# Kernel optimization log

Measured on AMD Instinct MI355X. Metric: run time of the kernel, lower is better.

Reference implementation:

```python
import jax, jax.numpy as jnp
import numpy as np

N_NODES = 50000
N_EDGES = 600000
HIDDEN = 128


def setup_inputs() -> dict:
    key = jax.random.key(0)
    ks = jax.random.split(key, 8)
    x = jax.random.normal(ks[0], (N_NODES, HIDDEN), dtype=jnp.float32)
    edge_index = jax.random.randint(ks[1], (2, N_EDGES), 0, N_NODES, dtype=jnp.int32)
    s = 1.0 / np.sqrt(HIDDEN)
    # PyG SAGEConv: lin_l applied to aggregated neighbors (with bias), lin_r to root (no bias)
    W1l = jax.random.uniform(ks[2], (HIDDEN, HIDDEN), jnp.float32, -s, s)
    b1l = jax.random.uniform(ks[3], (HIDDEN,), jnp.float32, -s, s)
    W1r = jax.random.uniform(ks[4], (HIDDEN, HIDDEN), jnp.float32, -s, s)
    W2l = jax.random.uniform(ks[5], (HIDDEN, HIDDEN), jnp.float32, -s, s)
    b2l = jax.random.uniform(ks[6], (HIDDEN,), jnp.float32, -s, s)
    W2r = jax.random.uniform(ks[7], (HIDDEN, HIDDEN), jnp.float32, -s, s)
    return {"x": x, "edge_index": edge_index, "W1l": W1l, "b1l": b1l,
            "W1r": W1r, "W2l": W2l, "b2l": b2l, "W2r": W2r}


def _sage_conv(x, src, dst, Wl, bl, Wr):
    # mean aggregation of source features at destination nodes
    msg_sum = jax.ops.segment_sum(x[src], dst, num_segments=N_NODES)  # [N, H]
    deg = jax.ops.segment_sum(jnp.ones((src.shape[0],), x.dtype), dst,
                              num_segments=N_NODES)  # [N]
    agg = msg_sum / jnp.maximum(deg, 1.0)[:, None]
    return agg @ Wl.T + bl + x @ Wr.T


def reference(x, edge_index, W1l, b1l, W1r, W2l, b2l, W2r):
    src, dst = edge_index[0], edge_index[1]
    h = jax.nn.relu(_sage_conv(x, src, dst, W1l, b1l, W1r))
    out = _sage_conv(h, src, dst, W2l, b2l, W2r)
    return out
```

## Files before the change

kernel.cpp:

```cpp
#include <hip/hip_runtime.h>
#include <hip/hip_bf16.h>

#define N_NODES 50000
#define N_EDGES 600000
#define HID 128
#define SCAN_BLOCKS ((N_NODES + 255) / 256)

typedef __attribute__((ext_vector_type(8))) __bf16 bf16x8;
typedef __attribute__((ext_vector_type(4))) float f32x4;

static __device__ __forceinline__ unsigned short f2b(float v) {
    return __builtin_bit_cast(unsigned short, (__bf16)v);
}


__global__ void k_deg(const int* __restrict__ dst, int* __restrict__ fill, int ne) {
    int e = blockIdx.x * blockDim.x + threadIdx.x;
    if (e < ne) atomicAdd(&fill[dst[e]], 1);
}

__global__ __launch_bounds__(256) void k_bsum(const int* __restrict__ fill, int* __restrict__ bsum, int n) {
    __shared__ int s[256];
    int tid = threadIdx.x;
    int i = blockIdx.x * 256 + tid;
    s[tid] = (i < n) ? fill[i] : 0;
    __syncthreads();
#pragma unroll
    for (int off = 128; off > 0; off >>= 1) {
        if (tid < off) s[tid] += s[tid + off];
        __syncthreads();
    }
    if (tid == 0) bsum[blockIdx.x] = s[0];
}

__global__ __launch_bounds__(256) void k_scan_bsum(int* __restrict__ bsum, int* __restrict__ row_off,
                                                   int nb, int n) {
    __shared__ int s[256];
    int tid = threadIdx.x;
    int v = (tid < nb) ? bsum[tid] : 0;
    s[tid] = v;
    __syncthreads();
#pragma unroll
    for (int off = 1; off < 256; off <<= 1) {
        int t = (tid >= off) ? s[tid - off] : 0;
        __syncthreads();
        s[tid] += t;
        __syncthreads();
    }
    if (tid < nb) bsum[tid] = s[tid] - v;
    if (tid == 255) row_off[n] = s[255];
}

__global__ __launch_bounds__(256) void k_write_off(int* __restrict__ fill, const int* __restrict__ bsum,
                                                   int* __restrict__ row_off, float* __restrict__ inv_deg,
                                                   int n) {
    __shared__ int s[256];
    int tid = threadIdx.x;
    int i = blockIdx.x * 256 + tid;
    int c = (i < n) ? fill[i] : 0;
    s[tid] = c;
    __syncthreads();
#pragma unroll
    for (int off = 1; off < 256; off <<= 1) {
        int t = (tid >= off) ? s[tid - off] : 0;
        __syncthreads();
        s[tid] += t;
        __syncthreads();
    }
    if (i < n) {
        row_off[i] = bsum[blockIdx.x] + s[tid] - c;
        inv_deg[i] = 1.0f / (float)max(c, 1);
        fill[i] = 0;
    }
}

__global__ void k_place(const int* __restrict__ src, const int* __restrict__ dst,
                        const int* __restrict__ row_off, int* __restrict__ fill,
                        int* __restrict__ csr, int ne) {
    int e = blockIdx.x * blockDim.x + threadIdx.x;
    if (e < ne) {
        int d = dst[e];
        int pos = atomicAdd(&fill[d], 1);
        csr[row_off[d] + pos] = src[e];
    }
}


__global__ void k_cast(const float* __restrict__ x, unsigned short* __restrict__ xb, int n4) {
    int i = blockIdx.x * blockDim.x + threadIdx.x;
    if (i >= n4) return;
    float4 v = *(const float4*)(x + (size_t)i * 4);
    ushort4 o;
    o.x = f2b(v.x); o.y = f2b(v.y); o.z = f2b(v.z); o.w = f2b(v.w);
    *(ushort4*)(xb + (size_t)i * 4) = o;
}


__global__ void k_prepV(const float* __restrict__ W1l, const float* __restrict__ W1r,
                        const float* __restrict__ W2l, const float* __restrict__ W2r,
                        unsigned short* __restrict__ V1, unsigned short* __restrict__ V2) {
    int idx = blockIdx.x * blockDim.x + threadIdx.x;
    if (idx >= 2 * 128 * 256) return;
    int which = idx >> 15;
    int i = idx & 32767;
    int j = i >> 8, k = i & 255;
    const float* Wl = which ? W2l : W1l;
    const float* Wr = which ? W2r : W1r;
    float v = (k < HID) ? Wl[j * HID + k] : Wr[j * HID + k - HID];
    (which ? V2 : V1)[i] = f2b(v);
}


static __device__ __forceinline__ void acc_bf2(uint2 v, float& a0, float& a1, float& a2, float& a3) {
    a0 += __uint_as_float(v.x << 16);
    a1 += __uint_as_float(v.x & 0xffff0000u);
    a2 += __uint_as_float(v.y << 16);
    a3 += __uint_as_float(v.y & 0xffff0000u);
}

__global__ __launch_bounds__(256) void k_agg(const unsigned short* __restrict__ xb,
                                             const int* __restrict__ csr,
                                             const int* __restrict__ row_off,
                                             const float* __restrict__ inv_deg,
                                             unsigned short* __restrict__ aggB, int n) {
    int g = (blockIdx.x * blockDim.x + threadIdx.x) >> 5;
    int lane = threadIdx.x & 31;
    if (g >= n) return;
    int e0 = row_off[g], e1 = row_off[g + 1];
    float a0 = 0.f, a1 = 0.f, a2 = 0.f, a3 = 0.f;
    int e = e0;
    for (; e + 4 <= e1; e += 4) {
        int s0 = csr[e + 0];
        int s1 = csr[e + 1];
        int s2 = csr[e + 2];
        int s3 = csr[e + 3];
        uint2 v0 = *(const uint2*)(xb + (size_t)s0 * HID + lane * 4);
        uint2 v1 = *(const uint2*)(xb + (size_t)s1 * HID + lane * 4);
        uint2 v2 = *(const uint2*)(xb + (size_t)s2 * HID + lane * 4);
        uint2 v3 = *(const uint2*)(xb + (size_t)s3 * HID + lane * 4);
        acc_bf2(v0, a0, a1, a2, a3);
        acc_bf2(v1, a0, a1, a2, a3);
        acc_bf2(v2, a0, a1, a2, a3);
        acc_bf2(v3, a0, a1, a2, a3);
    }
    if (e + 2 <= e1) {
        int s0 = csr[e + 0];
        int s1 = csr[e + 1];
        uint2 v0 = *(const uint2*)(xb + (size_t)s0 * HID + lane * 4);
        uint2 v1 = *(const uint2*)(xb + (size_t)s1 * HID + lane * 4);
        acc_bf2(v0, a0, a1, a2, a3);
        acc_bf2(v1, a0, a1, a2, a3);
        e += 2;
    }
    if (e < e1) {
        int s0 = csr[e];
        uint2 v0 = *(const uint2*)(xb + (size_t)s0 * HID + lane * 4);
        acc_bf2(v0, a0, a1, a2, a3);
    }
    float inv = inv_deg[g];
    ushort4 o;
    o.x = f2b(a0 * inv); o.y = f2b(a1 * inv); o.z = f2b(a2 * inv); o.w = f2b(a3 * inv);
    *(ushort4*)(aggB + (size_t)g * HID + lane * 4) = o;
}


__global__ __launch_bounds__(512) void k_gemm(const unsigned short* __restrict__ aggB,
                                              const unsigned short* __restrict__ xinB,
                                              const unsigned short* __restrict__ VT,
                                              const float* __restrict__ bias,
                                              float* __restrict__ outF,
                                              unsigned short* __restrict__ outB,
                                              int mode ,
                                              int nrows) {
    __shared__ char As[32768];
    __shared__ char Bs[32768];
    int tid = threadIdx.x;
    int w = tid >> 6, l = tid & 63;
    int r0 = blockIdx.x * 128;

    f32x4 acc[8] = {};

    int arow = w * 16 + (l & 15);
    int kgrp = (l >> 4) * 8;

    for (int p = 0; p < 2; ++p) {
        const unsigned short* Asrc = p ? xinB : aggB;
#pragma unroll
        for (int q = 0; q < 4; ++q) {
            int c = tid + q * 512;
            int m = c >> 4, c16 = c & 15;
            int gr = r0 + m;
            uint4 v = make_uint4(0, 0, 0, 0);
            if (gr < nrows) v = *(const uint4*)(Asrc + (size_t)gr * HID + c16 * 8);
            int byt = (m * 256 + c16 * 16) ^ ((m & 7) << 4);
            *(uint4*)(As + byt) = v;
        }
#pragma unroll
        for (int q = 0; q < 4; ++q) {
            int c = tid + q * 512;
            int j = c >> 4, c16 = c & 15;
            uint4 v = *(const uint4*)(VT + (size_t)j * 256 + p * 128 + c16 * 8);
            int byt = (j * 256 + c16 * 16) ^ ((j & 7) << 4);
            *(uint4*)(Bs + byt) = v;
        }
        __syncthreads();

#pragma unroll
        for (int s = 0; s < 4; ++s) {
            int koff = (s * 32 + kgrp) * 2;
            bf16x8 a = *(const bf16x8*)(As + ((arow * 256 + koff) ^ ((arow & 7) << 4)));
#pragma unroll
            for (int cc = 0; cc < 8; ++cc) {
                int brow = cc * 16 + (l & 15);
                bf16x8 b = *(const bf16x8*)(Bs + ((brow * 256 + koff) ^ ((brow & 7) << 4)));
                acc[cc] = __builtin_amdgcn_mfma_f32_16x16x32_bf16(a, b, acc[cc], 0, 0, 0);
            }
        }
        __syncthreads();
    }

    int lo = l & 15, hi = l >> 4;
#pragma unroll
    for (int cc = 0; cc < 8; ++cc) {
        int col = cc * 16 + lo;
        float bv = bias[col];
#pragma unroll
        for (int i = 0; i < 4; ++i) {
            int gr = r0 + w * 16 + hi * 4 + i;
            if (gr < nrows) {
                float v = acc[cc][i] + bv;
                if (mode) {
                    v = fmaxf(v, 0.f);
                    outB[(size_t)gr * HID + col] = f2b(v);
                } else {
                    outF[(size_t)gr * HID + col] = v;
                }
            }
        }
    }
}


extern "C" void kernel_launch(void* const* d_in, const int* in_sizes, int n_in,
                              void* d_out, int out_size, void* d_ws, size_t ws_size,
                              hipStream_t stream) {
    const float* x   = (const float*)d_in[0];
    const int*   ei  = (const int*)d_in[1];
    const float* W1l = (const float*)d_in[2];
    const float* b1l = (const float*)d_in[3];
    const float* W1r = (const float*)d_in[4];
    const float* W2l = (const float*)d_in[5];
    const float* b2l = (const float*)d_in[6];
    const float* W2r = (const float*)d_in[7];
    float* out = (float*)d_out;

    const int* src = ei;
    const int* dst = ei + N_EDGES;

    char* w = (char*)d_ws;
    unsigned short* aggB = (unsigned short*)(w);
    unsigned short* buf0 = (unsigned short*)(w + 12800000);
    int*   csr     = (int*)(w + 25600000);
    int*   row_off = (int*)(w + 28000000);
    int*   fill    = (int*)(w + 28200192);
    float* inv_deg = (float*)(w + 28400384);
    unsigned short* V1 = (unsigned short*)(w + 28600576);
    unsigned short* V2 = (unsigned short*)(w + 28666112);
    int*   bsum    = (int*)(w + 28731648);

    hipMemsetAsync(fill, 0, N_NODES * sizeof(int), stream);
    k_deg<<<(N_EDGES + 255) / 256, 256, 0, stream>>>(dst, fill, N_EDGES);
    k_bsum<<<SCAN_BLOCKS, 256, 0, stream>>>(fill, bsum, N_NODES);
    k_scan_bsum<<<1, 256, 0, stream>>>(bsum, row_off, SCAN_BLOCKS, N_NODES);
    k_write_off<<<SCAN_BLOCKS, 256, 0, stream>>>(fill, bsum, row_off, inv_deg, N_NODES);
    k_place<<<(N_EDGES + 255) / 256, 256, 0, stream>>>(src, dst, row_off, fill, csr, N_EDGES);

    k_prepV<<<(2 * 128 * 256 + 255) / 256, 256, 0, stream>>>(W1l, W1r, W2l, W2r, V1, V2);
    k_cast<<<(N_NODES * HID / 4 + 255) / 256, 256, 0, stream>>>(x, buf0, N_NODES * HID / 4);

    const int gemm_grid = (N_NODES + 127) / 128;

    k_agg<<<(N_NODES * 32 + 255) / 256, 256, 0, stream>>>(buf0, csr, row_off, inv_deg, aggB, N_NODES);
    k_gemm<<<gemm_grid, 512, 0, stream>>>(aggB, buf0, V1, b1l, out, buf0, 1, N_NODES);

    k_agg<<<(N_NODES * 32 + 255) / 256, 256, 0, stream>>>(buf0, csr, row_off, inv_deg, aggB, N_NODES);
    k_gemm<<<gemm_grid, 512, 0, stream>>>(aggB, buf0, V2, b2l, out, buf0, 0, N_NODES);
}
```

Baseline: 165.9 us.

## Fuse neighbor aggregation into GEMM and merge prep and scan kernels

New measurement: 297.8 us. 1.79x slower.

```diff
diff --git a/kernel.cpp b/kernel.cpp
--- a/kernel.cpp
+++ b/kernel.cpp
@@ -4,13 +4,59 @@
 #define N_NODES 50000
 #define N_EDGES 600000
 #define HID 128
-#define SCAN_BLOCKS ((N_NODES + 255) / 256)
 
 typedef __attribute__((ext_vector_type(8))) __bf16 bf16x8;
 typedef __attribute__((ext_vector_type(4))) float f32x4;
 
 static __device__ __forceinline__ unsigned short f2b(float v) {
     return __builtin_bit_cast(unsigned short, (__bf16)v);
+}
+
+
+#define NCAST (N_NODES * HID / 8)
+#define NVT   (2 * 128 * 256 / 8)
+#define NFILL (N_NODES / 4)
+#define NPREP (NCAST + NVT + NFILL)
+
+__global__ __launch_bounds__(256) void k_prep(const float* __restrict__ x,
+                                              const float* __restrict__ W1l, const float* __restrict__ W1r,
+                                              const float* __restrict__ W2l, const float* __restrict__ W2r,
+                                              unsigned short* __restrict__ xb,
+                                              unsigned short* __restrict__ V1,
+                                              unsigned short* __restrict__ V2,
+                                              int* __restrict__ fill) {
+    int idx = blockIdx.x * 256 + threadIdx.x;
+    if (idx < NCAST) {
+        const float4* xp = (const float4*)(x + (size_t)idx * 8);
+        float4 a = xp[0], b = xp[1];
+        uint4 o;
+        o.x = f2b(a.x) | ((unsigned)f2b(a.y) << 16);
+        o.y = f2b(a.z) | ((unsigned)f2b(a.w) << 16);
+        o.z = f2b(b.x) | ((unsigned)f2b(b.y) << 16);
+        o.w = f2b(b.z) | ((unsigned)f2b(b.w) << 16);
+        *(uint4*)(xb + (size_t)idx * 8) = o;
+    } else if (idx < NCAST + NVT) {
+        int t = idx - NCAST;
+        int i0 = t * 8;
+        int which = i0 >> 15;
+        const float* Wl = which ? W2l : W1l;
+        const float* Wr = which ? W2r : W1r;
+        unsigned short* V = which ? V2 : V1;
+        int ii = i0 & 32767;
+        int j = ii >> 8, k0 = ii & 255;
+        const float* Wp = (k0 < HID) ? (Wl + j * HID + k0) : (Wr + j * HID + (k0 - HID));
+        const float4* wp4 = (const float4*)Wp;
+        float4 a = wp4[0], b = wp4[1];
+        uint4 o;
+        o.x = f2b(a.x) | ((unsigned)f2b(a.y) << 16);
+        o.y = f2b(a.z) | ((unsigned)f2b(a.w) << 16);
+        o.z = f2b(b.x) | ((unsigned)f2b(b.y) << 16);
+        o.w = f2b(b.z) | ((unsigned)f2b(b.w) << 16);
+        *(uint4*)(V + ii) = o;
+    } else if (idx < NPREP) {
+        int z = idx - (NCAST + NVT);
+        *(int4*)(fill + z * 4) = make_int4(0, 0, 0, 0);
+    }
 }
 
 
@@ -19,59 +65,33 @@
     if (e < ne) atomicAdd(&fill[dst[e]], 1);
 }
 
-__global__ __launch_bounds__(256) void k_bsum(const int* __restrict__ fill, int* __restrict__ bsum, int n) {
-    __shared__ int s[256];
+#define SCAN_T 1024
+#define SCAN_PER ((N_NODES + SCAN_T - 1) / SCAN_T)
+
+__global__ __launch_bounds__(1024) void k_scan1(int* __restrict__ fill, int* __restrict__ row_off,
+                                                float* __restrict__ inv_deg, int n) {
+    __shared__ int s[SCAN_T];
     int tid = threadIdx.x;
-    int i = blockIdx.x * 256 + tid;
-    s[tid] = (i < n) ? fill[i] : 0;
-    __syncthreads();
-#pragma unroll
-    for (int off = 128; off > 0; off >>= 1) {
-        if (tid < off) s[tid] += s[tid + off];
-        __syncthreads();
-    }
-    if (tid == 0) bsum[blockIdx.x] = s[0];
-}
-
-__global__ __launch_bounds__(256) void k_scan_bsum(int* __restrict__ bsum, int* __restrict__ row_off,
-                                                   int nb, int n) {
-    __shared__ int s[256];
-    int tid = threadIdx.x;
-    int v = (tid < nb) ? bsum[tid] : 0;
-    s[tid] = v;
-    __syncthreads();
-#pragma unroll
-    for (int off = 1; off < 256; off <<= 1) {
+    int s0 = tid * SCAN_PER, s1 = min(s0 + SCAN_PER, n);
+    int sum = 0;
+    for (int i = s0; i < s1; ++i) sum += fill[i];
+    s[tid] = sum;
+    __syncthreads();
+    for (int off = 1; off < SCAN_T; off <<= 1) {
         int t = (tid >= off) ? s[tid - off] : 0;
         __syncthreads();
         s[tid] += t;
         __syncthreads();
     }
-    if (tid < nb) bsum[tid] = s[tid] - v;
-    if (tid == 255) row_off[n] = s[255];
-}
-
-__global__ __launch_bounds__(256) void k_write_off(int* __restrict__ fill, const int* __restrict__ bsum,
-                                                   int* __restrict__ row_off, float* __restrict__ inv_deg,
-                                                   int n) {
-    __shared__ int s[256];
-    int tid = threadIdx.x;
-    int i = blockIdx.x * 256 + tid;
-    int c = (i < n) ? fill[i] : 0;
-    s[tid] = c;
-    __syncthreads();
-#pragma unroll
-    for (int off = 1; off < 256; off <<= 1) {
-        int t = (tid >= off) ? s[tid - off] : 0;
-        __syncthreads();
-        s[tid] += t;
-        __syncthreads();
-    }
-    if (i < n) {
-        row_off[i] = bsum[blockIdx.x] + s[tid] - c;
+    int run = s[tid] - sum;
+    for (int i = s0; i < s1; ++i) {
+        int c = fill[i];
+        row_off[i] = run;
         inv_deg[i] = 1.0f / (float)max(c, 1);
+        run += c;
         fill[i] = 0;
     }
+    if (tid == 0) row_off[n] = N_EDGES;
 }
 
 __global__ void k_place(const int* __restrict__ src, const int* __restrict__ dst,
@@ -86,31 +106,6 @@
 }
 
 
-__global__ void k_cast(const float* __restrict__ x, unsigned short* __restrict__ xb, int n4) {
-    int i = blockIdx.x * blockDim.x + threadIdx.x;
-    if (i >= n4) return;
-    float4 v = *(const float4*)(x + (size_t)i * 4);
-    ushort4 o;
-    o.x = f2b(v.x); o.y = f2b(v.y); o.z = f2b(v.z); o.w = f2b(v.w);
-    *(ushort4*)(xb + (size_t)i * 4) = o;
-}
-
-
-__global__ void k_prepV(const float* __restrict__ W1l, const float* __restrict__ W1r,
-                        const float* __restrict__ W2l, const float* __restrict__ W2r,
-                        unsigned short* __restrict__ V1, unsigned short* __restrict__ V2) {
-    int idx = blockIdx.x * blockDim.x + threadIdx.x;
-    if (idx >= 2 * 128 * 256) return;
-    int which = idx >> 15;
-    int i = idx & 32767;
-    int j = i >> 8, k = i & 255;
-    const float* Wl = which ? W2l : W1l;
-    const float* Wr = which ? W2r : W1r;
-    float v = (k < HID) ? Wl[j * HID + k] : Wr[j * HID + k - HID];
-    (which ? V2 : V1)[i] = f2b(v);
-}
-
-
 static __device__ __forceinline__ void acc_bf2(uint2 v, float& a0, float& a1, float& a2, float& a3) {
     a0 += __uint_as_float(v.x << 16);
     a1 += __uint_as_float(v.x & 0xffff0000u);
@@ -118,56 +113,12 @@
     a3 += __uint_as_float(v.y & 0xffff0000u);
 }
 
-__global__ __launch_bounds__(256) void k_agg(const unsigned short* __restrict__ xb,
-                                             const int* __restrict__ csr,
-                                             const int* __restrict__ row_off,
-                                             const float* __restrict__ inv_deg,
-                                             unsigned short* __restrict__ aggB, int n) {
-    int g = (blockIdx.x * blockDim.x + threadIdx.x) >> 5;
-    int lane = threadIdx.x & 31;
-    if (g >= n) return;
-    int e0 = row_off[g], e1 = row_off[g + 1];
-    float a0 = 0.f, a1 = 0.f, a2 = 0.f, a3 = 0.f;
-    int e = e0;
-    for (; e + 4 <= e1; e += 4) {
-        int s0 = csr[e + 0];
-        int s1 = csr[e + 1];
-        int s2 = csr[e + 2];
-        int s3 = csr[e + 3];
-        uint2 v0 = *(const uint2*)(xb + (size_t)s0 * HID + lane * 4);
-        uint2 v1 = *(const uint2*)(xb + (size_t)s1 * HID + lane * 4);
-        uint2 v2 = *(const uint2*)(xb + (size_t)s2 * HID + lane * 4);
-        uint2 v3 = *(const uint2*)(xb + (size_t)s3 * HID + lane * 4);
-        acc_bf2(v0, a0, a1, a2, a3);
-        acc_bf2(v1, a0, a1, a2, a3);
-        acc_bf2(v2, a0, a1, a2, a3);
-        acc_bf2(v3, a0, a1, a2, a3);
-    }
-    if (e + 2 <= e1) {
-        int s0 = csr[e + 0];
-        int s1 = csr[e + 1];
-        uint2 v0 = *(const uint2*)(xb + (size_t)s0 * HID + lane * 4);
-        uint2 v1 = *(const uint2*)(xb + (size_t)s1 * HID + lane * 4);
-        acc_bf2(v0, a0, a1, a2, a3);
-        acc_bf2(v1, a0, a1, a2, a3);
-        e += 2;
-    }
-    if (e < e1) {
-        int s0 = csr[e];
-        uint2 v0 = *(const uint2*)(xb + (size_t)s0 * HID + lane * 4);
-        acc_bf2(v0, a0, a1, a2, a3);
-    }
-    float inv = inv_deg[g];
-    ushort4 o;
-    o.x = f2b(a0 * inv); o.y = f2b(a1 * inv); o.z = f2b(a2 * inv); o.w = f2b(a3 * inv);
-    *(ushort4*)(aggB + (size_t)g * HID + lane * 4) = o;
-}
-
-
-__global__ __launch_bounds__(512) void k_gemm(const unsigned short* __restrict__ aggB,
-                                              const unsigned short* __restrict__ xinB,
+__global__ __launch_bounds__(512) void k_gemm(const unsigned short* __restrict__ srcF,
                                               const unsigned short* __restrict__ VT,
                                               const float* __restrict__ bias,
+                                              const int* __restrict__ csr,
+                                              const int* __restrict__ row_off,
+                                              const float* __restrict__ inv_deg,
                                               float* __restrict__ outF,
                                               unsigned short* __restrict__ outB,
                                               int mode ,
@@ -179,44 +130,108 @@
     int r0 = blockIdx.x * 128;
 
     f32x4 acc[8] = {};
-
     int arow = w * 16 + (l & 15);
     int kgrp = (l >> 4) * 8;
 
-    for (int p = 0; p < 2; ++p) {
-        const unsigned short* Asrc = p ? xinB : aggB;
-#pragma unroll
-        for (int q = 0; q < 4; ++q) {
-            int c = tid + q * 512;
-            int m = c >> 4, c16 = c & 15;
-            int gr = r0 + m;
-            uint4 v = make_uint4(0, 0, 0, 0);
-            if (gr < nrows) v = *(const uint4*)(Asrc + (size_t)gr * HID + c16 * 8);
-            int byt = (m * 256 + c16 * 16) ^ ((m & 7) << 4);
-            *(uint4*)(As + byt) = v;
-        }
-#pragma unroll
-        for (int q = 0; q < 4; ++q) {
-            int c = tid + q * 512;
-            int j = c >> 4, c16 = c & 15;
-            uint4 v = *(const uint4*)(VT + (size_t)j * 256 + p * 128 + c16 * 8);
-            int byt = (j * 256 + c16 * 16) ^ ((j & 7) << 4);
-            *(uint4*)(Bs + byt) = v;
-        }
-        __syncthreads();
-
-#pragma unroll
-        for (int s = 0; s < 4; ++s) {
-            int koff = (s * 32 + kgrp) * 2;
-            bf16x8 a = *(const bf16x8*)(As + ((arow * 256 + koff) ^ ((arow & 7) << 4)));
-#pragma unroll
-            for (int cc = 0; cc < 8; ++cc) {
-                int brow = cc * 16 + (l & 15);
-                bf16x8 b = *(const bf16x8*)(Bs + ((brow * 256 + koff) ^ ((brow & 7) << 4)));
-                acc[cc] = __builtin_amdgcn_mfma_f32_16x16x32_bf16(a, b, acc[cc], 0, 0, 0);
+#pragma unroll
+    for (int q = 0; q < 4; ++q) {
+        int c = tid + q * 512;
+        int jr = c >> 4, c16 = c & 15;
+        uint4 v = *(const uint4*)(VT + (size_t)jr * 256 + c16 * 8);
+        int byt = (jr * 256 + c16 * 16) ^ ((jr & 7) << 4);
+        *(uint4*)(Bs + byt) = v;
+    }
+
+    {
+        int g = tid >> 5;
+        int lane = tid & 31;
+#pragma unroll 1
+        for (int j = 0; j < 8; ++j) {
+            int m = g * 8 + j;
+            int node = r0 + m;
+            float a0 = 0.f, a1 = 0.f, a2 = 0.f, a3 = 0.f;
+            if (node < nrows) {
+                int e0 = row_off[node], e1 = row_off[node + 1];
+                int e = e0;
+                for (; e + 4 <= e1; e += 4) {
+                    int i0 = csr[e + 0], i1 = csr[e + 1], i2 = csr[e + 2], i3 = csr[e + 3];
+                    uint2 v0 = *(const uint2*)(srcF + (size_t)i0 * HID + lane * 4);
+                    uint2 v1 = *(const uint2*)(srcF + (size_t)i1 * HID + lane * 4);
+                    uint2 v2 = *(const uint2*)(srcF + (size_t)i2 * HID + lane * 4);
+                    uint2 v3 = *(const uint2*)(srcF + (size_t)i3 * HID + lane * 4);
+                    acc_bf2(v0, a0, a1, a2, a3);
+                    acc_bf2(v1, a0, a1, a2, a3);
+                    acc_bf2(v2, a0, a1, a2, a3);
+                    acc_bf2(v3, a0, a1, a2, a3);
+                }
+                if (e + 2 <= e1) {
+                    int i0 = csr[e + 0], i1 = csr[e + 1];
+                    uint2 v0 = *(const uint2*)(srcF + (size_t)i0 * HID + lane * 4);
+                    uint2 v1 = *(const uint2*)(srcF + (size_t)i1 * HID + lane * 4);
+                    acc_bf2(v0, a0, a1, a2, a3);
+                    acc_bf2(v1, a0, a1, a2, a3);
+                    e += 2;
+                }
+                if (e < e1) {
+                    int i0 = csr[e];
+                    uint2 v0 = *(const uint2*)(srcF + (size_t)i0 * HID + lane * 4);
+                    acc_bf2(v0, a0, a1, a2, a3);
+                }
+                float inv = inv_deg[node];
+                a0 *= inv; a1 *= inv; a2 *= inv; a3 *= inv;
             }
-        }
-        __syncthreads();
+            uint2 o;
+            o.x = f2b(a0) | ((unsigned)f2b(a1) << 16);
+            o.y = f2b(a2) | ((unsigned)f2b(a3) << 16);
+            int byt = (m * 256 + lane * 8) ^ ((m & 7) << 4);
+            *(uint2*)(As + byt) = o;
+        }
+    }
+    __syncthreads();
+
+#pragma unroll
+    for (int s = 0; s < 4; ++s) {
+        int koff = (s * 32 + kgrp) * 2;
+        bf16x8 a = *(const bf16x8*)(As + ((arow * 256 + koff) ^ ((arow & 7) << 4)));
+#pragma unroll
+        for (int cc = 0; cc < 8; ++cc) {
+            int brow = cc * 16 + (l & 15);
+            bf16x8 b = *(const bf16x8*)(Bs + ((brow * 256 + koff) ^ ((brow & 7) << 4)));
+            acc[cc] = __builtin_amdgcn_mfma_f32_16x16x32_bf16(a, b, acc[cc], 0, 0, 0);
+        }
+    }
+    __syncthreads();
+
+#pragma unroll
+    for (int q = 0; q < 4; ++q) {
+        int c = tid + q * 512;
+        int m = c >> 4, c16 = c & 15;
+        int gr = r0 + m;
+        uint4 v = make_uint4(0, 0, 0, 0);
+        if (gr < nrows) v = *(const uint4*)(srcF + (size_t)gr * HID + c16 * 8);
+        int byt = (m * 256 + c16 * 16) ^ ((m & 7) << 4);
+        *(uint4*)(As + byt) = v;
+    }
+#pragma unroll
+    for (int q = 0; q < 4; ++q) {
+        int c = tid + q * 512;
+        int jr = c >> 4, c16 = c & 15;
+        uint4 v = *(const uint4*)(VT + (size_t)jr * 256 + 128 + c16 * 8);
+        int byt = (jr * 256 + c16 * 16) ^ ((jr & 7) << 4);
+        *(uint4*)(Bs + byt) = v;
+    }
+    __syncthreads();
+
+#pragma unroll
+    for (int s = 0; s < 4; ++s) {
+        int koff = (s * 32 + kgrp) * 2;
+        bf16x8 a = *(const bf16x8*)(As + ((arow * 256 + koff) ^ ((arow & 7) << 4)));
+#pragma unroll
+        for (int cc = 0; cc < 8; ++cc) {
+            int brow = cc * 16 + (l & 15);
+            bf16x8 b = *(const bf16x8*)(Bs + ((brow * 256 + koff) ^ ((brow & 7) << 4)));
+            acc[cc] = __builtin_amdgcn_mfma_f32_16x16x32_bf16(a, b, acc[cc], 0, 0, 0);
+        }
     }
 
     int lo = l & 15, hi = l >> 4;
@@ -258,31 +273,26 @@
     const int* dst = ei + N_EDGES;
 
     char* w = (char*)d_ws;
-    unsigned short* aggB = (unsigned short*)(w);
-    unsigned short* buf0 = (unsigned short*)(w + 12800000);
+    unsigned short* hb  = (unsigned short*)(w);
+    unsigned short* xb  = (unsigned short*)(w + 12800000);
     int*   csr     = (int*)(w + 25600000);
     int*   row_off = (int*)(w + 28000000);
     int*   fill    = (int*)(w + 28200192);
     float* inv_deg = (float*)(w + 28400384);
     unsigned short* V1 = (unsigned short*)(w + 28600576);
     unsigned short* V2 = (unsigned short*)(w + 28666112);
-    int*   bsum    = (int*)(w + 28731648);
-
-    hipMemsetAsync(fill, 0, N_NODES * sizeof(int), stream);
+
+    k_prep<<<(NPREP + 255) / 256, 256, 0, stream>>>(x, W1l, W1r, W2l, W2r, xb, V1, V2, fill);
+
     k_deg<<<(N_EDGES + 255) / 256, 256, 0, stream>>>(dst, fill, N_EDGES);
-    k_bsum<<<SCAN_BLOCKS, 256, 0, stream>>>(fill, bsum, N_NODES);
-    k_scan_bsum<<<1, 256, 0, stream>>>(bsum, row_off, SCAN_BLOCKS, N_NODES);
-    k_write_off<<<SCAN_BLOCKS, 256, 0, stream>>>(fill, bsum, row_off, inv_deg, N_NODES);
+
+    k_scan1<<<1, SCAN_T, 0, stream>>>(fill, row_off, inv_deg, N_NODES);
+
     k_place<<<(N_EDGES + 255) / 256, 256, 0, stream>>>(src, dst, row_off, fill, csr, N_EDGES);
 
-    k_prepV<<<(2 * 128 * 256 + 255) / 256, 256, 0, stream>>>(W1l, W1r, W2l, W2r, V1, V2);
-    k_cast<<<(N_NODES * HID / 4 + 255) / 256, 256, 0, stream>>>(x, buf0, N_NODES * HID / 4);
-
     const int gemm_grid = (N_NODES + 127) / 128;
 
-    k_agg<<<(N_NODES * 32 + 255) / 256, 256, 0, stream>>>(buf0, csr, row_off, inv_deg, aggB, N_NODES);
-    k_gemm<<<gemm_grid, 512, 0, stream>>>(aggB, buf0, V1, b1l, out, buf0, 1, N_NODES);
-
-    k_agg<<<(N_NODES * 32 + 255) / 256, 256, 0, stream>>>(buf0, csr, row_off, inv_deg, aggB, N_NODES);
-    k_gemm<<<gemm_grid, 512, 0, stream>>>(aggB, buf0, V2, b2l, out, buf0, 0, N_NODES);
-}
+    k_gemm<<<gemm_grid, 512, 0, stream>>>(xb, V1, b1l, csr, row_off, inv_deg, out, hb, 1, N_NODES);
+
+    k_gemm<<<gemm_grid, 512, 0, stream>>>(hb, V2, b2l, csr, row_off, inv_deg, out, hb, 0, N_NODES);
+}
```
